# Kernel tuning notes

Hardware: AMD Instinct MI355X
Metric: run time of the kernel (lower is better)

Reference implementation:

```python
import jax, jax.numpy as jnp
import numpy as np


def _scan_dir(x, Wk, Wr, b):
    # x: (B,H,W,C) already flipped for the direction; Wk:(C,4U) Wr:(U,4U) b:(4U,)
    B, H, W, C = x.shape
    U = Wr.shape[0]
    Dmax = min(H, W)          # max anti-diagonal length
    D = H + W - 1             # number of anti-diagonals
    dt = x.dtype
    k = jnp.arange(Dmax)

    def step(carry, d):
        h1, c1, h2, c2 = carry            # diag d-1 and d-2 buffers, (B,Dmax,U)
        i0 = jnp.maximum(0, d - (W - 1))  # first row on diag d
        i1 = jnp.minimum(H - 1, d)        # last row on diag d
        rows = i0 + k
        cols = d - rows
        mask = rows <= i1                 # valid lanes on this diagonal
        rs = jnp.clip(rows, 0, H - 1)
        cs = jnp.clip(cols, 0, W - 1)
        x_diag = x[:, rs, cs, :]          # (B,Dmax,C)
        i0p = jnp.maximum(0, d - W)       # i0 of diag d-1
        i0pp = jnp.maximum(0, d - 1 - W)  # i0 of diag d-2

        def nb(buf, r_nb, lane0, extra):
            v = mask & extra
            lane = jnp.clip(r_nb - lane0, 0, Dmax - 1)
            g = jnp.take(buf, lane, axis=1)
            return jnp.where(v[None, :, None], g, jnp.zeros_like(g)), v

        up_ok = rows - 1 >= 0
        left_ok = cols - 1 >= 0
        h_up, v_up = nb(h1, rows - 1, i0p, up_ok)        # (i-1, j)   on diag d-1
        h_left, v_left = nb(h1, rows, i0p, left_ok)      # (i, j-1)   on diag d-1
        h_ul, v_ul = nb(h2, rows - 1, i0pp, up_ok & left_ok)  # (i-1,j-1) diag d-2
        c_up, _ = nb(c1, rows - 1, i0p, up_ok)
        c_left, _ = nb(c1, rows, i0p, left_ok)
        c_ul, _ = nb(c2, rows - 1, i0pp, up_ok & left_ok)

        cnt = (v_up.astype(dt) + v_left.astype(dt) + v_ul.astype(dt))[None, :, None]
        cnt = jnp.maximum(cnt, jnp.asarray(1.0, dt))
        h_prev = (h_up + h_left + h_ul) / cnt
        c_prev = (c_up + c_left + c_ul) / cnt

        # keras LSTMCell math, gate order i,f,g,o
        z = x_diag @ Wk + h_prev @ Wr + b
        zi, zf, zg, zo = jnp.split(z, 4, axis=-1)
        c_new = jax.nn.sigmoid(zf) * c_prev + jax.nn.sigmoid(zi) * jnp.tanh(zg)
        h_new = jax.nn.sigmoid(zo) * jnp.tanh(c_new)
        m = mask[None, :, None]
        h_new = jnp.where(m, h_new, jnp.zeros_like(h_new))
        c_new = jnp.where(m, c_new, jnp.zeros_like(c_new))
        return (h_new, c_new, h1, c1), h_new

    z0 = jnp.zeros((B, Dmax, U), dt)
    _, hs = jax.lax.scan(step, (z0, z0, z0, z0), jnp.arange(D))  # (D,B,Dmax,U)

    # scatter diagonal buffers back into the (B,H,W,U) grid (static indices)
    d_arr = np.arange(D)[:, None]
    kk = np.arange(Dmax)[None, :]
    rows_all = np.maximum(0, d_arr - (W - 1)) + kk
    cols_all = d_arr - rows_all
    valid = rows_all <= np.minimum(H - 1, d_arr)
    rws = np.where(valid, rows_all, H)   # invalid lanes -> padding row H
    cws = np.where(valid, cols_all, 0)
    out = jnp.zeros((B, H + 1, W, U), dt)
    out = out.at[:, rws, cws].set(jnp.transpose(hs, (1, 0, 2, 3)))
    return out[:, :H]


_FLIPS = [(False, False), (False, True), (True, False), (True, True)]  # SE,SW,NE,NW


def _forward(x, Wk, Wr, b):
    outs = []
    for i, (fh, fw) in enumerate(_FLIPS):
        xx = x
        if fh:
            xx = xx[:, ::-1]
        if fw:
            xx = xx[:, :, ::-1]
        o = _scan_dir(xx, Wk[i], Wr[i], b[i])
        if fw:
            o = o[:, :, ::-1]
        if fh:
            o = o[:, ::-1]
        outs.append(o)
    return jnp.concatenate(outs, axis=-1)


def setup_inputs() -> dict:
    key = jax.random.key(0)
    k0, k1, k2, k3 = jax.random.split(key, 4)
    B, H, W, C, U = 4, 128, 128, 64, 64
    x = jax.random.normal(k0, (B, H, W, C), jnp.float32)
    Wk = jax.random.normal(k1, (4, C, 4 * U), jnp.float32) * 0.08
    Wr = jax.random.normal(k2, (4, U, 4 * U), jnp.float32) * 0.08
    b = jax.random.normal(k3, (4, 4 * U), jnp.float32) * 0.02
    return {"x": x, "Wk": Wk, "Wr": Wr, "b": b}


def reference(x, Wk, Wr, b):
    return _forward(x, Wk, Wr, b)
```

## Files before the change

kernel.cpp:

```cpp
#include <hip/hip_runtime.h>

typedef __bf16 bf16x8 __attribute__((ext_vector_type(8)));
typedef __bf16 bf16x4 __attribute__((ext_vector_type(4)));
typedef float f32x4 __attribute__((ext_vector_type(4)));
typedef unsigned long long u64;

#define NCH 8
#define CELLS 16
#define NG 256
#define L2E 1.44269504089f
#define RDEPTH 16
#define NLINK (16 * 7)
#define RING_U64 (NLINK * RDEPTH * 64)
#define PROG_OFF (RING_U64 * 8)

__device__ __forceinline__ unsigned short f2bfbits(float f) {
  __bf16 b = (__bf16)f;
  return __builtin_bit_cast(unsigned short, b);
}
__device__ __forceinline__ float bfbits2f(unsigned short s) {
  return (float)__builtin_bit_cast(__bf16, s);
}
__device__ __forceinline__ void barrier_lds() {
  asm volatile("s_waitcnt lgkmcnt(0)" ::: "memory");
  __builtin_amdgcn_s_barrier();
}
__device__ __forceinline__ int hix(int row, int byteoff) {
  return row * 128 + (byteoff ^ ((row & 7) << 4));
}

__global__ __launch_bounds__(512, 1) void mdrnn_kernel(
    const float* __restrict__ x, const float* __restrict__ Wk,
    const float* __restrict__ Wr, const float* __restrict__ bias,
    float* __restrict__ out, char* __restrict__ ws) {
  __shared__ __align__(16) unsigned char xt[3][CELLS * 128];
  __shared__ __align__(16) unsigned char Pbuf[2][CELLS * 128];
  __shared__ __align__(16) unsigned char gbh[8 * 128];
  __shared__ __align__(16) float gbc[8 * 64];
  __shared__ __align__(16) float zbuf[2][4096];

  u64* __restrict__ ring = (u64*)ws;
  int* __restrict__ prog = (int*)(ws + PROG_OFF);

  const int tid = threadIdx.x;
  const bool isComp = (tid < 256);
  const int L = tid & 63;
  const int lo16 = L & 15;
  const int hi16 = L >> 4;
  const int wq = (tid >> 6) & 3;
  const int u = wq * 16 + lo16;
  const int hm0 = (tid >> 4) & 15;
  const int hq16 = tid & 15;

  const int ch = blockIdx.x >> 4;
  const int g = blockIdx.x & 15;
  const int f = g >> 2;
  const int bb = g & 3;
  const int fh = (f >> 1) & 1;
  const int fw = f & 1;
  const int R0 = ch * CELLS;
  const int D1 = R0 + 142;
  const int linkDn = g * 7 + ch - 1;
  const int linkUp = g * 7 + ch;

  for (int i = tid; i < 3 * CELLS * 32; i += 512) ((int*)xt)[i] = 0;
  for (int i = tid; i < 2 * CELLS * 32; i += 512) ((int*)Pbuf)[i] = 0;
  for (int i = tid; i < 8 * 32; i += 512) ((int*)gbh)[i] = 0;
  for (int i = tid; i < 8 * 64; i += 512) gbc[i] = 0.f;

  float bsc[4] = {0.f, 0.f, 0.f, 0.f};
  bf16x8 wkh[4][2], wrh[4][2], wrl[4][2];
  int oidx[4];
  int oStep = 0, cbase = 0;
  int o_ph0 = 0, o_ph1 = 0;
  int o_pw[4] = {0, 0, 0, 0};
  if (isComp) {
    const float* Wrf = Wr + f * (64 * NG);
#pragma unroll
    for (int t = 0; t < 4; ++t) {
      const float st = (t == 2) ? (2.f * L2E) : L2E;
#pragma unroll
      for (int kt = 0; kt < 2; ++kt)
#pragma unroll
        for (int jj = 0; jj < 8; ++jj) {
          int k = kt * 32 + hi16 * 8 + jj;
          float vr = Wrf[k * NG + t * 64 + u] * st;
          __bf16 vh = (__bf16)vr;
          wrh[t][kt][jj] = vh;
          wrl[t][kt][jj] = (__bf16)(vr - (float)vh);
        }
    }
    const int ccStep = fw ? -1 : 1;
#pragma unroll
    for (int j = 0; j < 4; ++j) {
      int ro = R0 + hi16 * 4 + j;
      int rr = fh ? 127 - ro : ro;
      int c0 = R0 - ro;
      oidx[j] = ((bb * 128 + rr) * 128 + (fw ? 127 - c0 : c0)) * NG + f * 64 + u;
      o_pw[j] = hix(hi16 * 4 + j, u * 2);
    }
    oStep = ccStep * NG;
    cbase = -hi16 * 4;
    o_ph0 = hix(lo16, hi16 * 16);
    o_ph1 = hix(lo16, 64 + hi16 * 16);
  } else {
    const float* Wkf = Wk + f * (64 * NG);
#pragma unroll
    for (int t = 0; t < 4; ++t) {
      const float st = (t == 2) ? (2.f * L2E) : L2E;
      bsc[t] = bias[f * NG + t * 64 + u] * st;
#pragma unroll
      for (int kt = 0; kt < 2; ++kt)
#pragma unroll
        for (int jj = 0; jj < 8; ++jj) {
          int k = kt * 32 + hi16 * 8 + jj;
          wkh[t][kt][jj] = (__bf16)(Wkf[k * NG + t * 64 + u] * st);
        }
    }
  }
  const int o_ax0 = hix(lo16, hi16 * 16);
  const int o_ax1 = hix(lo16, 64 + hi16 * 16);

  const int ccStepH = fw ? -1 : 1;
  const int rx = R0 + hm0;
  const int rrx = fh ? 127 - rx : rx;
  int cx = R0 - rx;
  int xidx = ((bb * 128 + rrx) * 128 + (fw ? 127 - cx : cx)) * 64 + hq16 * 4;
  const int xStep = ccStepH * 64;
  float4 px;
  bool pxv = false;
  auto ldg = [&]() {
    pxv = ((unsigned)cx <= 127u);
    px = make_float4(0.f, 0.f, 0.f, 0.f);
    if (pxv) px = *(const float4*)(x + xidx);
    xidx += xStep;
    ++cx;
  };
  auto stx = [&](unsigned char* buf) {
    if (pxv) {
      bf16x4 pk;
      pk[0] = (__bf16)px.x; pk[1] = (__bf16)px.y;
      pk[2] = (__bf16)px.z; pk[3] = (__bf16)px.w;
      *(bf16x4*)(buf + hix(hm0, hq16 * 8)) = pk;
    }
  };
  auto accx = [&](const unsigned char* xp, int bi) {
    bf16x8 a0 = *(const bf16x8*)(xp + o_ax0);
    bf16x8 a1 = *(const bf16x8*)(xp + o_ax1);
    float* zw = &zbuf[bi][0] + (wq * 64 + L) * 4;
#pragma unroll
    for (int t = 0; t < 4; ++t) {
      f32x4 az = (f32x4){bsc[t], bsc[t], bsc[t], bsc[t]};
      az = __builtin_amdgcn_mfma_f32_16x16x32_bf16(a0, wkh[t][0], az, 0, 0, 0);
      az = __builtin_amdgcn_mfma_f32_16x16x32_bf16(a1, wkh[t][1], az, 0, 0, 0);
      *(f32x4*)(zw + t * 1024) = az;
    }
  };

  __syncthreads();

  if (!isComp) {
    ldg();
    stx(&xt[R0 % 3][0]);
    ldg();
  }
  __syncthreads();

  if (!isComp) {
    stx(&xt[(R0 + 1) % 3][0]);
    ldg();
    accx(&xt[R0 % 3][0], R0 & 1);
    if (wq == 0 && ch > 0) {
#pragma unroll
      for (int k = 0; k < 2; ++k) {
        const int q = R0 - 1 + k;
        u64* src = ring + ((linkDn * RDEPTH + (q & (RDEPTH - 1))) << 6) + L;
        u64 v;
        int spin = 0;
        for (;;) {
          v = __hip_atomic_load(src, __ATOMIC_RELAXED, __HIP_MEMORY_SCOPE_AGENT);
          if ((unsigned short)(v >> 48) == (unsigned short)q ||
              spin >= (1 << 22))
            break;
          ++spin;
          __builtin_amdgcn_s_sleep(2);
        }
        *(unsigned short*)(gbh + (q & 7) * 128 + L * 2) =
            (unsigned short)(v >> 32);
        gbc[(q & 7) * 64 + L] = __uint_as_float((unsigned)v);
        if (k == 0)
          *(unsigned short*)(&Pbuf[(R0 + 1) & 1][0] + L * 2) =
              (unsigned short)(v >> 32);
      }
      if (L == 0)
        __hip_atomic_store(&prog[linkDn * 16], R0, __ATOMIC_RELAXED,
                           __HIP_MEMORY_SCOPE_AGENT);
    }
  }
  __syncthreads();

  f32x4 zacc[4];
  float hnprev[4];
  float cnv[4];
  float csj[4];
  float puv[4];
  int gateSeen = 0;
  if (isComp) {
    const float* zb = &zbuf[R0 & 1][0] + (wq * 64 + L) * 4;
#pragma unroll
    for (int t = 0; t < 4; ++t) zacc[t] = *(const f32x4*)(zb + t * 1024);
    const float cu0 = gbc[((R0 - 1) & 7) * 64 + u];
#pragma unroll
    for (int j = 0; j < 4; ++j) {
      const float ci = (hi16 == 0 && j == 0) ? cu0 : 0.f;
      csj[j] = ci;
      puv[j] = ci;
      hnprev[j] = 0.f;
      cnv[j] = 0.f;
    }
    __builtin_amdgcn_s_setprio(1);
  } else {
    accx(&xt[(R0 + 1) % 3][0], (R0 + 1) & 1);
    stx(&xt[(R0 + 2) % 3][0]);
    ldg();
  }
  __syncthreads();

  unsigned char* Pc = &Pbuf[R0 & 1][0];
  unsigned char* Pp = &Pbuf[(R0 + 1) & 1][0];
  unsigned char* xA = &xt[(R0 + 2) % 3][0];
  unsigned char* xB = &xt[R0 % 3][0];
  unsigned char* xC = &xt[(R0 + 1) % 3][0];

  for (int d = R0; d <= D1; ++d) {
    if (isComp) {
      bf16x8 pa0 = *(const bf16x8*)(Pp + o_ph0);
      bf16x8 pa1 = *(const bf16x8*)(Pp + o_ph1);
#pragma unroll
      for (int t = 0; t < 4; ++t)
        zacc[t] = __builtin_amdgcn_mfma_f32_16x16x32_bf16(pa0, wrh[t][0], zacc[t], 0, 0, 0);
#pragma unroll
      for (int t = 0; t < 4; ++t)
        zacc[t] = __builtin_amdgcn_mfma_f32_16x16x32_bf16(pa1, wrh[t][1], zacc[t], 0, 0, 0);
#pragma unroll
      for (int t = 0; t < 4; ++t)
        zacc[t] = __builtin_amdgcn_mfma_f32_16x16x32_bf16(pa0, wrl[t][0], zacc[t], 0, 0, 0);
#pragma unroll
      for (int t = 0; t < 4; ++t)
        zacc[t] = __builtin_amdgcn_mfma_f32_16x16x32_bf16(pa1, wrl[t][1], zacc[t], 0, 0, 0);

      const bool pub = (ch < NCH - 1) && (d >= R0 + 15);
      if (pub && d >= R0 + 15 + RDEPTH && gateSeen < d - RDEPTH)
        gateSeen = __hip_atomic_load(&prog[linkUp * 16], __ATOMIC_RELAXED,
                                     __HIP_MEMORY_SCOPE_AGENT);

      const float gh1 = bfbits2f(*(const unsigned short*)(gbh + (d & 7) * 128 + u * 2));
      const float gh2 = bfbits2f(*(const unsigned short*)(gbh + ((d - 1) & 7) * 128 + u * 2));
      const float gc1 = gbc[(d & 7) * 64 + u];

      float hcur[4], cnew[4];
#pragma unroll
      for (int jj = 0; jj < 4; ++jj) {
        const int j = 3 - jj;
        const int lm = hi16 * 4 + j;
        const int cj = cbase - j;
        const bool ok = ((unsigned)cj <= 127u);
        const float inv = (cj == 0 || (R0 + lm) == 0) ? 1.f : (1.f / 3.f);
        const float cpj = csj[j] * inv;
        const float e1 = __builtin_amdgcn_exp2f(-zacc[1][j]);
        const float e2 = __builtin_amdgcn_exp2f(-zacc[0][j]);
        const float e3 = __builtin_amdgcn_exp2f(zacc[2][j]);
        float cn = cpj * __builtin_amdgcn_rcpf(1.f + e1) +
                   (e3 - 1.f) * __builtin_amdgcn_rcpf((1.f + e2) * (1.f + e3));
        const float e4 = __builtin_amdgcn_exp2f(-zacc[3][j]);
        const float e5 = __builtin_amdgcn_exp2f(2.f * L2E * cn);
        float hn = (e5 - 1.f) * __builtin_amdgcn_rcpf((1.f + e4) * (1.f + e5));
        if (pub && lm == CELLS - 1) {
          if (d >= R0 + 15 + RDEPTH && gateSeen < d - RDEPTH) {
            int spin = 0;
            do {
              gateSeen = __hip_atomic_load(&prog[linkUp * 16], __ATOMIC_RELAXED,
                                           __HIP_MEMORY_SCOPE_AGENT);
            } while (gateSeen < d - RDEPTH && ++spin < (1 << 22));
          }
          u64 v = ((u64)(unsigned short)d << 48) | ((u64)f2bfbits(hn) << 32) |
                  (u64)__float_as_uint(cn);
          u64* dst = ring + ((linkUp * RDEPTH + (d & (RDEPTH - 1))) << 6) + u;
          __hip_atomic_store(dst, v, __ATOMIC_RELAXED,
                             __HIP_MEMORY_SCOPE_AGENT);
        }
        hn = ok ? hn : 0.f;
        cn = ok ? cn : 0.f;
        hcur[j] = hn;
        cnew[j] = cn;
        if (ok) out[oidx[j]] = hn;
      }

      const unsigned pk =
          ((unsigned)f2bfbits(hcur[3]) << 16) | f2bfbits(hnprev[3]);
      const unsigned pku = __shfl((int)pk, (L - 16) & 63);
      const float up_h = bfbits2f((unsigned short)(pku >> 16));
      const float up_hp = bfbits2f((unsigned short)(pku & 0xffff));
      const float up_c = __shfl(cnew[3], (L - 16) & 63);
#pragma unroll
      for (int j = 0; j < 4; ++j) {
        const float hup = j ? hcur[j - 1] : (hi16 ? up_h : gh1);
        const float hulp = j ? hnprev[j - 1] : (hi16 ? up_hp : gh2);
        const float sPj =
            ((cbase + 1 == j) || (R0 == 0 && hi16 == 0 && j == 0))
                ? 1.f : (1.f / 3.f);
        *(unsigned short*)(Pc + o_pw[j]) =
            f2bfbits(sPj * (hup + hcur[j] + hulp));
        const float cun = j ? cnew[j - 1] : (hi16 ? up_c : gc1);
        csj[j] = cun + cnew[j] + puv[j];
        puv[j] = cun;
      }
#pragma unroll
      for (int j = 0; j < 4; ++j) {
        hnprev[j] = hcur[j];
        cnv[j] = cnew[j];
        oidx[j] += oStep;
      }
      ++cbase;

      const float* zb = &zbuf[(d + 1) & 1][0] + (wq * 64 + L) * 4;
#pragma unroll
      for (int t = 0; t < 4; ++t) zacc[t] = *(const f32x4*)(zb + t * 1024);
    } else {
      const bool doPoll = (((d - R0) & 1) == 0) && (ch > 0) && (wq == 0);
      u64 pv[3];
      const u64* ps[3];
      bool live[3];
      if (doPoll) {
        const int kk0 = (d == R0) ? 0 : 1;
#pragma unroll
        for (int k = 0; k < 3; ++k) {
          const int q = d + 1 + k;
          live[k] = (k >= kk0) && (q <= R0 + 126);
          ps[k] = ring + ((linkDn * RDEPTH + (q & (RDEPTH - 1))) << 6) + L;
          pv[k] = live[k] ? __hip_atomic_load(ps[k], __ATOMIC_RELAXED,
                                              __HIP_MEMORY_SCOPE_AGENT)
                          : 0;
        }
      }
      accx(xA, (d + 2) & 1);
      stx(xB);
      ldg();
      if (doPoll) {
#pragma unroll
        for (int k = 0; k < 3; ++k) {
          if (!live[k]) continue;
          const int q = d + 1 + k;
          int spin = 0;
          while ((unsigned short)(pv[k] >> 48) != (unsigned short)q &&
                 spin < (1 << 22)) {
            ++spin;
            __builtin_amdgcn_s_sleep(1);
            pv[k] = __hip_atomic_load(ps[k], __ATOMIC_RELAXED,
                                      __HIP_MEMORY_SCOPE_AGENT);
          }
          *(unsigned short*)(gbh + (q & 7) * 128 + L * 2) =
              (unsigned short)(pv[k] >> 32);
          gbc[(q & 7) * 64 + L] = __uint_as_float((unsigned)pv[k]);
        }
        if (L == 0)
          __hip_atomic_store(&prog[linkDn * 16], min(d + 3, R0 + 126),
                             __ATOMIC_RELAXED, __HIP_MEMORY_SCOPE_AGENT);
      }
    }

    {
      unsigned char* t0 = xA; xA = xB; xB = xC; xC = t0;
      unsigned char* t1 = Pc; Pc = Pp; Pp = t1;
    }
    barrier_lds();
  }
}

extern "C" void kernel_launch(void* const* d_in, const int* in_sizes, int n_in,
                              void* d_out, int out_size, void* d_ws, size_t ws_size,
                              hipStream_t stream) {
  const float* x = (const float*)d_in[0];
  const float* Wk = (const float*)d_in[1];
  const float* Wr = (const float*)d_in[2];
  const float* b = (const float*)d_in[3];
  float* out = (float*)d_out;
  hipMemsetAsync(d_ws, 0, PROG_OFF + NLINK * 16 * sizeof(int), stream);
  hipLaunchKernelGGL(mdrnn_kernel, dim3(128), dim3(512), 0, stream, x, Wk, Wr,
                     b, out, (char*)d_ws);
}
```

Baseline: 268.6 us.

## Offload ring publishing to producer warps and pipeline consumer polling per step

Compute warps no longer publish boundary h/c to the global ring or spin on the downstream gate. They write the packed value to a double-buffered LDS slot, and a producer warp stores it to the ring one step later, after the barrier. The critical lane-3 cell is computed first so its shuffles can overlap the other cells. Polling for incoming boundary data now alternates between two producer warps, fetching one entry three steps ahead, and the prologue prefetches four entries. This takes global atomics and spin loops off the recurrent critical path, at the cost of one extra step of publish latency across chunks.

```diff
diff --git a/kernel.cpp b/kernel.cpp
--- a/kernel.cpp
+++ b/kernel.cpp
@@ -38,6 +38,7 @@
   __shared__ __align__(16) unsigned char gbh[8 * 128];
   __shared__ __align__(16) float gbc[8 * 64];
   __shared__ __align__(16) float zbuf[2][4096];
+  __shared__ __align__(16) u64 pubbuf[2][64];
 
   u64* __restrict__ ring = (u64*)ws;
   int* __restrict__ prog = (int*)(ws + PROG_OFF);
@@ -172,7 +173,7 @@
     accx(&xt[R0 % 3][0], R0 & 1);
     if (wq == 0 && ch > 0) {
 #pragma unroll
-      for (int k = 0; k < 2; ++k) {
+      for (int k = 0; k < 4; ++k) {
         const int q = R0 - 1 + k;
         u64* src = ring + ((linkDn * RDEPTH + (q & (RDEPTH - 1))) << 6) + L;
         u64 v;
@@ -193,7 +194,7 @@
               (unsigned short)(v >> 32);
       }
       if (L == 0)
-        __hip_atomic_store(&prog[linkDn * 16], R0, __ATOMIC_RELAXED,
+        __hip_atomic_store(&prog[linkDn * 16], R0 + 2, __ATOMIC_RELAXED,
                            __HIP_MEMORY_SCOPE_AGENT);
     }
   }
@@ -201,7 +202,6 @@
 
   f32x4 zacc[4];
   float hnprev[4];
-  float cnv[4];
   float csj[4];
   float puv[4];
   int gateSeen = 0;
@@ -216,7 +216,6 @@
       csj[j] = ci;
       puv[j] = ci;
       hnprev[j] = 0.f;
-      cnv[j] = 0.f;
     }
     __builtin_amdgcn_s_setprio(1);
   } else {
@@ -236,32 +235,56 @@
     if (isComp) {
       bf16x8 pa0 = *(const bf16x8*)(Pp + o_ph0);
       bf16x8 pa1 = *(const bf16x8*)(Pp + o_ph1);
-#pragma unroll
-      for (int t = 0; t < 4; ++t)
-        zacc[t] = __builtin_amdgcn_mfma_f32_16x16x32_bf16(pa0, wrh[t][0], zacc[t], 0, 0, 0);
-#pragma unroll
-      for (int t = 0; t < 4; ++t)
-        zacc[t] = __builtin_amdgcn_mfma_f32_16x16x32_bf16(pa1, wrh[t][1], zacc[t], 0, 0, 0);
-#pragma unroll
-      for (int t = 0; t < 4; ++t)
-        zacc[t] = __builtin_amdgcn_mfma_f32_16x16x32_bf16(pa0, wrl[t][0], zacc[t], 0, 0, 0);
-#pragma unroll
-      for (int t = 0; t < 4; ++t)
-        zacc[t] = __builtin_amdgcn_mfma_f32_16x16x32_bf16(pa1, wrl[t][1], zacc[t], 0, 0, 0);
-
-      const bool pub = (ch < NCH - 1) && (d >= R0 + 15);
-      if (pub && d >= R0 + 15 + RDEPTH && gateSeen < d - RDEPTH)
-        gateSeen = __hip_atomic_load(&prog[linkUp * 16], __ATOMIC_RELAXED,
-                                     __HIP_MEMORY_SCOPE_AGENT);
-
       const float gh1 = bfbits2f(*(const unsigned short*)(gbh + (d & 7) * 128 + u * 2));
       const float gh2 = bfbits2f(*(const unsigned short*)(gbh + ((d - 1) & 7) * 128 + u * 2));
       const float gc1 = gbc[(d & 7) * 64 + u];
+#pragma unroll
+      for (int t = 0; t < 4; ++t)
+        zacc[t] = __builtin_amdgcn_mfma_f32_16x16x32_bf16(pa0, wrh[t][0], zacc[t], 0, 0, 0);
+#pragma unroll
+      for (int t = 0; t < 4; ++t)
+        zacc[t] = __builtin_amdgcn_mfma_f32_16x16x32_bf16(pa1, wrh[t][1], zacc[t], 0, 0, 0);
+#pragma unroll
+      for (int t = 0; t < 4; ++t)
+        zacc[t] = __builtin_amdgcn_mfma_f32_16x16x32_bf16(pa0, wrl[t][0], zacc[t], 0, 0, 0);
+#pragma unroll
+      for (int t = 0; t < 4; ++t)
+        zacc[t] = __builtin_amdgcn_mfma_f32_16x16x32_bf16(pa1, wrl[t][1], zacc[t], 0, 0, 0);
+
+      const bool pubW = (ch < NCH - 1) && (d >= R0 + 15);
 
       float hcur[4], cnew[4];
-#pragma unroll
-      for (int jj = 0; jj < 4; ++jj) {
-        const int j = 3 - jj;
+      {
+        const int lm = hi16 * 4 + 3;
+        const int cj = cbase - 3;
+        const bool ok = ((unsigned)cj <= 127u);
+        const float inv = (cj == 0 || (R0 + lm) == 0) ? 1.f : (1.f / 3.f);
+        const float cpj = csj[3] * inv;
+        const float e1 = __builtin_amdgcn_exp2f(-zacc[1][3]);
+        const float e2 = __builtin_amdgcn_exp2f(-zacc[0][3]);
+        const float e3 = __builtin_amdgcn_exp2f(zacc[2][3]);
+        float cn = cpj * __builtin_amdgcn_rcpf(1.f + e1) +
+                   (e3 - 1.f) * __builtin_amdgcn_rcpf((1.f + e2) * (1.f + e3));
+        const float e4 = __builtin_amdgcn_exp2f(-zacc[3][3]);
+        const float e5 = __builtin_amdgcn_exp2f(2.f * L2E * cn);
+        float hn = (e5 - 1.f) * __builtin_amdgcn_rcpf((1.f + e4) * (1.f + e5));
+        if (pubW && lm == CELLS - 1)
+          pubbuf[d & 1][u] = ((u64)(unsigned short)d << 48) |
+                             ((u64)f2bfbits(hn) << 32) |
+                             (u64)__float_as_uint(cn);
+        hn = ok ? hn : 0.f;
+        cn = ok ? cn : 0.f;
+        hcur[3] = hn;
+        cnew[3] = cn;
+        if (ok) out[oidx[3]] = hn;
+      }
+      const unsigned pk =
+          ((unsigned)f2bfbits(hcur[3]) << 16) | f2bfbits(hnprev[3]);
+      const unsigned pku = __shfl((int)pk, (L - 16) & 63);
+      const float up_c = __shfl(cnew[3], (L - 16) & 63);
+#pragma unroll
+      for (int jj = 0; jj < 3; ++jj) {
+        const int j = 2 - jj;
         const int lm = hi16 * 4 + j;
         const int cj = cbase - j;
         const bool ok = ((unsigned)cj <= 127u);
@@ -275,33 +298,15 @@
         const float e4 = __builtin_amdgcn_exp2f(-zacc[3][j]);
         const float e5 = __builtin_amdgcn_exp2f(2.f * L2E * cn);
         float hn = (e5 - 1.f) * __builtin_amdgcn_rcpf((1.f + e4) * (1.f + e5));
-        if (pub && lm == CELLS - 1) {
-          if (d >= R0 + 15 + RDEPTH && gateSeen < d - RDEPTH) {
-            int spin = 0;
-            do {
-              gateSeen = __hip_atomic_load(&prog[linkUp * 16], __ATOMIC_RELAXED,
-                                           __HIP_MEMORY_SCOPE_AGENT);
-            } while (gateSeen < d - RDEPTH && ++spin < (1 << 22));
-          }
-          u64 v = ((u64)(unsigned short)d << 48) | ((u64)f2bfbits(hn) << 32) |
-                  (u64)__float_as_uint(cn);
-          u64* dst = ring + ((linkUp * RDEPTH + (d & (RDEPTH - 1))) << 6) + u;
-          __hip_atomic_store(dst, v, __ATOMIC_RELAXED,
-                             __HIP_MEMORY_SCOPE_AGENT);
-        }
         hn = ok ? hn : 0.f;
         cn = ok ? cn : 0.f;
         hcur[j] = hn;
         cnew[j] = cn;
         if (ok) out[oidx[j]] = hn;
       }
-
-      const unsigned pk =
-          ((unsigned)f2bfbits(hcur[3]) << 16) | f2bfbits(hnprev[3]);
-      const unsigned pku = __shfl((int)pk, (L - 16) & 63);
       const float up_h = bfbits2f((unsigned short)(pku >> 16));
       const float up_hp = bfbits2f((unsigned short)(pku & 0xffff));
-      const float up_c = __shfl(cnew[3], (L - 16) & 63);
+
 #pragma unroll
       for (int j = 0; j < 4; ++j) {
         const float hup = j ? hcur[j - 1] : (hi16 ? up_h : gh1);
@@ -318,7 +323,6 @@
 #pragma unroll
       for (int j = 0; j < 4; ++j) {
         hnprev[j] = hcur[j];
-        cnv[j] = cnew[j];
         oidx[j] += oStep;
       }
       ++cbase;
@@ -327,46 +331,50 @@
 #pragma unroll
       for (int t = 0; t < 4; ++t) zacc[t] = *(const f32x4*)(zb + t * 1024);
     } else {
-      const bool doPoll = (((d - R0) & 1) == 0) && (ch > 0) && (wq == 0);
-      u64 pv[3];
-      const u64* ps[3];
-      bool live[3];
-      if (doPoll) {
-        const int kk0 = (d == R0) ? 0 : 1;
-#pragma unroll
-        for (int k = 0; k < 3; ++k) {
-          const int q = d + 1 + k;
-          live[k] = (k >= kk0) && (q <= R0 + 126);
-          ps[k] = ring + ((linkDn * RDEPTH + (q & (RDEPTH - 1))) << 6) + L;
-          pv[k] = live[k] ? __hip_atomic_load(ps[k], __ATOMIC_RELAXED,
-                                              __HIP_MEMORY_SCOPE_AGENT)
-                          : 0;
+      const bool meAct = (ch > 0) && (wq == ((d - R0) & 1));
+      const int q = d + 3;
+      const bool qLive = meAct && (q <= R0 + 126);
+      const u64* qs = ring + ((linkDn * RDEPTH + (q & (RDEPTH - 1))) << 6) + L;
+      u64 qv = 0;
+      if (qLive)
+        qv = __hip_atomic_load(qs, __ATOMIC_RELAXED, __HIP_MEMORY_SCOPE_AGENT);
+
+      if (wq == 0 && ch < NCH - 1) {
+        const int pd = d - 1;
+        if (pd >= R0 + 15) {
+          if (pd >= R0 + 15 + RDEPTH && gateSeen < pd - RDEPTH) {
+            int spin = 0;
+            do {
+              gateSeen = __hip_atomic_load(&prog[linkUp * 16], __ATOMIC_RELAXED,
+                                           __HIP_MEMORY_SCOPE_AGENT);
+              if (gateSeen < pd - RDEPTH) __builtin_amdgcn_s_sleep(1);
+            } while (gateSeen < pd - RDEPTH && ++spin < (1 << 22));
+          }
+          u64 v = pubbuf[(d - 1) & 1][L];
+          u64* dst = ring + ((linkUp * RDEPTH + (pd & (RDEPTH - 1))) << 6) + L;
+          __hip_atomic_store(dst, v, __ATOMIC_RELAXED,
+                             __HIP_MEMORY_SCOPE_AGENT);
         }
       }
       accx(xA, (d + 2) & 1);
       stx(xB);
       ldg();
-      if (doPoll) {
-#pragma unroll
-        for (int k = 0; k < 3; ++k) {
-          if (!live[k]) continue;
-          const int q = d + 1 + k;
-          int spin = 0;
-          while ((unsigned short)(pv[k] >> 48) != (unsigned short)q &&
-                 spin < (1 << 22)) {
-            ++spin;
-            __builtin_amdgcn_s_sleep(1);
-            pv[k] = __hip_atomic_load(ps[k], __ATOMIC_RELAXED,
-                                      __HIP_MEMORY_SCOPE_AGENT);
-          }
-          *(unsigned short*)(gbh + (q & 7) * 128 + L * 2) =
-              (unsigned short)(pv[k] >> 32);
-          gbc[(q & 7) * 64 + L] = __uint_as_float((unsigned)pv[k]);
+      if (qLive) {
+        int spin = 0;
+        while ((unsigned short)(qv >> 48) != (unsigned short)q &&
+               spin < (1 << 22)) {
+          ++spin;
+          __builtin_amdgcn_s_sleep(1);
+          qv = __hip_atomic_load(qs, __ATOMIC_RELAXED,
+                                 __HIP_MEMORY_SCOPE_AGENT);
         }
-        if (L == 0)
-          __hip_atomic_store(&prog[linkDn * 16], min(d + 3, R0 + 126),
-                             __ATOMIC_RELAXED, __HIP_MEMORY_SCOPE_AGENT);
-      }
+        *(unsigned short*)(gbh + (q & 7) * 128 + L * 2) =
+            (unsigned short)(qv >> 32);
+        gbc[(q & 7) * 64 + L] = __uint_as_float((unsigned)qv);
+      }
+      if (meAct && L == 0)
+        __hip_atomic_store(&prog[linkDn * 16], min(d + 3, R0 + 126),
+                           __ATOMIC_RELAXED, __HIP_MEMORY_SCOPE_AGENT);
     }
 
     {
@@ -374,6 +382,21 @@
       unsigned char* t1 = Pc; Pc = Pp; Pp = t1;
     }
     barrier_lds();
+  }
+
+  if (!isComp && wq == 0 && ch < NCH - 1) {
+    const int pd = D1;
+    if (pd >= R0 + 15 + RDEPTH && gateSeen < pd - RDEPTH) {
+      int spin = 0;
+      do {
+        gateSeen = __hip_atomic_load(&prog[linkUp * 16], __ATOMIC_RELAXED,
+                                     __HIP_MEMORY_SCOPE_AGENT);
+        if (gateSeen < pd - RDEPTH) __builtin_amdgcn_s_sleep(1);
+      } while (gateSeen < pd - RDEPTH && ++spin < (1 << 22));
+    }
+    u64 v = pubbuf[D1 & 1][L];
+    u64* dst = ring + ((linkUp * RDEPTH + (pd & (RDEPTH - 1))) << 6) + L;
+    __hip_atomic_store(dst, v, __ATOMIC_RELAXED, __HIP_MEMORY_SCOPE_AGENT);
   }
 }
 
```

New measurement: 260.7 us. 3.0% less time.
